# Kernel tuning notes

Hardware: AMD Instinct MI355X
Metric: run time of the kernel (lower is better)

## Reference

```python
import jax, jax.numpy as jnp
import numpy as np

B, L, D = 8, 8192, 1024
M = L // 4  # target_ratio=4 -> exactly L/4 boundaries per batch row (enforced in setup_inputs)


@jax.custom_vjp
def ste(x):
    # Forward: ones_like(x). Backward: pass gradient straight through.
    return jnp.ones_like(x)

def _ste_fwd(x):
    return jnp.ones_like(x), None

def _ste_bwd(_, g):
    return (g,)

ste.defvjp(_ste_fwd, _ste_bwd)


def _ema_combine(c1, c2):
    # Linear recurrence h = a*h_prev + b as an associative op (matches the
    # Hillis-Steele doubling scan in the torch source exactly).
    a1, b1 = c1
    a2, b2 = c2
    return (a1 * a2, a2[..., None] * b1 + b2)


def setup_inputs() -> dict:
    key = jax.random.key(0)
    k1, k2, k3, k4, k5 = jax.random.split(key, 5)
    x = jax.random.normal(k1, (B, L, D), jnp.float32)
    residual = jax.random.normal(k2, (B, L, D), jnp.float32)
    prob = jax.random.uniform(k3, (B, L), jnp.float32)
    # exactly M=L//4 True positions per row (random locations) -> static M
    r = jax.random.uniform(k4, (B, L))
    sel = jnp.argsort(r, axis=1)[:, :M]
    token_mask = jnp.zeros((B, L), bool).at[jnp.arange(B)[:, None], sel].set(True)
    state = jax.random.normal(k5, (B, D), jnp.float32)
    return {"x": x, "residual": residual, "prob": prob,
            "token_mask": token_mask, "state": state}


def reference(x, residual, prob, token_mask, state):
    # ---- Tokenizer: compact selected positions to the front (stable order) ----
    counts = token_mask.sum(axis=1)                       # (B,)
    order = jnp.argsort(~token_mask, axis=1)[:, :M]       # stable: True positions first, in order
    chunked = jnp.take_along_axis(x, order[:, :, None], axis=1)      # (B, M, D)
    chunk_probs = jnp.take_along_axis(prob, order, axis=1)           # (B, M)
    valid = jnp.arange(M)[None, :] < counts[:, None]                  # (B, M)
    chunk_probs = chunk_probs * valid                     # padded slots -> 0 (new_zeros semantics)

    # ---- EMA scan over compacted chunks ----
    decay = jnp.clip(1.0 - chunk_probs, 0.0, 1.0)         # (B, M)
    b = (1.0 - decay)[..., None] * chunked                # (B, M, D)
    b = b.at[:, 0].add(decay[:, 0, None] * state)         # fold initial state into b[0]
    _, ema = jax.lax.associative_scan(_ema_combine, (decay, b), axis=1)
    ema = ema * valid[..., None]

    # ---- DeTokenizer: scatter-expand back to (B, L, D) ----
    chunk_idx = jnp.cumsum(token_mask.astype(jnp.int32), axis=1) - 1  # (B, L)
    valid_pos = chunk_idx >= 0
    ci = jnp.clip(chunk_idx, 0, M - 1)
    long_states = jnp.take_along_axis(ema, ci[:, :, None], axis=1)    # (B, L, D)
    long_states = long_states * valid_pos[..., None]

    coef = ste(jnp.maximum(1.0 - prob, prob))             # forward: ones; bwd: STE
    long_states = long_states * coef[..., None]

    output = residual + long_states                       # (B, L, D)

    # new_state = last valid EMA value per batch (or carried-over state if empty)
    last = jnp.clip(counts - 1, 0, M - 1)
    new_state = jnp.take_along_axis(ema, last[:, None, None], axis=1)[:, 0]
    new_state = jnp.where((counts > 0)[:, None], new_state, state)
    return output, new_state
```

## Files before the change

kernel.cpp:

```cpp
#include <hip/hip_runtime.h>
#include <stdint.h>
#include <stddef.h>

#define B_ 8
#define L_ 8192
#define D_ 1024
#define M_ 2048
#define D4_ (D_/4)
#define TROWS_ 64
#define NTILE_ (L_/TROWS_)

typedef float f4 __attribute__((ext_vector_type(4)));

#define OFF_POS    ((size_t)0)
#define OFF_DEC    (OFF_POS  + (size_t)B_*M_*4)
#define OFF_A      (OFF_DEC  + (size_t)B_*M_*4)
#define OFF_CIT    (OFF_A    + (size_t)B_*NTILE_*4)
#define OFF_EZ     (OFF_CIT  + (size_t)B_*NTILE_*4)
#define OFF_HINIT  (OFF_EZ   + (size_t)B_*NTILE_*D_*4)
#define WS_TOTAL   (OFF_HINIT + (size_t)B_*NTILE_*D_*4)

__global__ __launch_bounds__(1024)
void compact_kernel(const void* __restrict__ mask_raw,
                    const float* __restrict__ prob,
                    int* __restrict__ pos,
                    float* __restrict__ dec,
                    int* __restrict__ ci_tile) {
    const int b = blockIdx.x;
    const int t = threadIdx.x;

    __shared__ int u8flag;
    if (t == 0) u8flag = 0;
    __syncthreads();
    {
        const uint32_t* mu = (const uint32_t*)mask_raw;
        uint32_t w0 = mu[t * 2], w1 = mu[t * 2 + 1];
        if (w0 > 1u || w1 > 1u) atomicOr(&u8flag, 1);
    }
    __syncthreads();
    const bool u8 = (u8flag != 0);

    int mv[8];
    const int base_l = t * 8;
    if (u8) {
        const uint8_t* mrow = (const uint8_t*)mask_raw + (size_t)b * L_;
        #pragma unroll
        for (int j = 0; j < 8; j++) mv[j] = mrow[base_l + j] ? 1 : 0;
    } else {
        const int* mrow = (const int*)mask_raw + (size_t)b * L_;
        #pragma unroll
        for (int j = 0; j < 8; j++) mv[j] = mrow[base_l + j] ? 1 : 0;
    }
    int tsum = 0;
    #pragma unroll
    for (int j = 0; j < 8; j++) tsum += mv[j];

    const int lane = t & 63, wid = t >> 6;
    int v = tsum;
    #pragma unroll
    for (int off = 1; off < 64; off <<= 1) {
        int n = __shfl_up(v, off, 64);
        if (lane >= off) v += n;
    }
    __shared__ int wsum[16];
    __shared__ int woff[16];
    if (lane == 63) wsum[wid] = v;
    __syncthreads();
    if (t < 16) {
        int acc = 0;
        for (int w = 0; w < t; w++) acc += wsum[w];
        woff[t] = acc;
    }
    __syncthreads();
    int run = (v - tsum) + woff[wid];

    const float* prow = prob + (size_t)b * L_;
    #pragma unroll
    for (int j = 0; j < 8; j++) {
        const int l = base_l + j;
        if (mv[j]) {
            float d = 1.0f - prow[l];
            d = fminf(fmaxf(d, 0.0f), 1.0f);
            pos[(size_t)b * M_ + run] = l;
            dec[(size_t)b * M_ + run] = d;
            run += 1;
        }
    }
    if ((t & 7) == 7) {
        const int k = (t + 1) >> 3;
        if (k < NTILE_) ci_tile[b * NTILE_ + k] = run - 1;
    }
}

__global__ __launch_bounds__(256)
void segend_kernel(const f4* __restrict__ x4,
                   const int* __restrict__ pos,
                   const float* __restrict__ dec,
                   const int* __restrict__ ci_tile,
                   f4* __restrict__ ez4,
                   float* __restrict__ Aseg) {
    const int blk = blockIdx.x;
    const int b = blk >> 7;
    const int k = blk & (NTILE_ - 1);
    const int t = threadIdx.x;

    const int mlo = (k == 0) ? 0 : ci_tile[b * NTILE_ + k] + 1;
    const int mhi = (k == NTILE_ - 1) ? (M_ - 1) : ci_tile[b * NTILE_ + k + 1];
    const int n = mhi - mlo + 1;

    __shared__ int   pl[TROWS_];
    __shared__ float dl[TROWS_];
    if (t < n) {
        pl[t] = pos[(size_t)b * M_ + mlo + t];
        dl[t] = dec[(size_t)b * M_ + mlo + t];
    }
    __syncthreads();

    f4 h = (f4)(0.0f);
    float A = 1.0f;
    if (n > 0) {
        const f4* xrow = x4 + (size_t)b * L_ * D4_;
        for (int g = 0; g < n; g += 8) {
            f4    xv[8];
            float dd[8];
            #pragma unroll
            for (int j = 0; j < 8; j++) {
                const int mm = g + j;
                const int mc = (mm < n) ? mm : 0;
                dd[j] = (mm < n) ? dl[mc] : 1.0f;
                xv[j] = xrow[(size_t)pl[mc] * D4_ + t];
            }
            #pragma unroll
            for (int j = 0; j < 8; j++) {
                h = dd[j] * h + (1.0f - dd[j]) * xv[j];
                A *= dd[j];
            }
        }
    }
    ez4[(size_t)blk * D4_ + t] = h;
    if (t == 0) Aseg[blk] = A;
}

__global__ __launch_bounds__(64)
void combine_kernel(const float* __restrict__ ez,
                    const float* __restrict__ Aseg,
                    const float* __restrict__ state,
                    float* __restrict__ hinit,
                    float* __restrict__ newstate) {
    const int b = blockIdx.x;
    const int ch = blockIdx.y * 64 + threadIdx.x;
    __shared__ float Al[NTILE_];
    for (int i = threadIdx.x; i < NTILE_; i += 64) Al[i] = Aseg[b * NTILE_ + i];
    __syncthreads();

    float c = state[(size_t)b * D_ + ch];
    for (int s0 = 0; s0 < NTILE_; s0 += 8) {
        float e[8];
        #pragma unroll
        for (int j = 0; j < 8; j++)
            e[j] = ez[((size_t)b * NTILE_ + s0 + j) * D_ + ch];
        #pragma unroll
        for (int j = 0; j < 8; j++) {
            hinit[((size_t)b * NTILE_ + s0 + j) * D_ + ch] = c;
            c = fmaf(Al[s0 + j], c, e[j]);
        }
    }
    newstate[(size_t)b * D_ + ch] = c;
}

__global__ __launch_bounds__(256)
void fused_kernel(const f4* __restrict__ x4,
                  const f4* __restrict__ res4,
                  const int* __restrict__ pos,
                  const float* __restrict__ dec,
                  const int* __restrict__ ci_tile,
                  const f4* __restrict__ hinit4,
                  f4* __restrict__ out4) {
    const int blk = blockIdx.x;
    const int b = blk >> 7;
    const int k = blk & (NTILE_ - 1);
    const int t = threadIdx.x;
    const int l0 = k * TROWS_;

    const int m0 = (k == 0) ? -1 : ci_tile[b * NTILE_ + k];

    __shared__ int   pl[TROWS_ + 2];
    __shared__ float dl[TROWS_ + 2];
    if (t < TROWS_ + 2) {
        const int mm = m0 + 1 + t;
        if (mm < M_) {
            pl[t] = pos[(size_t)b * M_ + mm];
            dl[t] = dec[(size_t)b * M_ + mm];
        } else {
            pl[t] = L_;
            dl[t] = 1.0f;
        }
    }
    __syncthreads();

    const f4* xrow = x4 + (size_t)b * L_ * D4_;

    f4 h = hinit4[(size_t)blk * D4_ + t];
    float live = (m0 >= 0) ? 1.0f : 0.0f;

    const f4* resrow = res4 + (size_t)b * L_ * D4_;
    f4*       outrow = out4 + (size_t)b * L_ * D4_;

    int mi = 0;
    int nextb = pl[0];
    int a0 = (pl[0] < L_) ? pl[0] : 0;
    int a1 = (pl[1] < L_) ? pl[1] : 0;
    f4 xn  = xrow[(size_t)a0 * D4_ + t];
    f4 xn2 = xrow[(size_t)a1 * D4_ + t];
    int l = l0;

    #define ADV(K, HH, LV)                                                \
        if (l + (K) == nextb) {                                           \
            const float d_ = dl[mi];                                      \
            h = d_ * h + (1.0f - d_) * xn;                                \
            live = 1.0f;                                                  \
            xn = xn2;                                                     \
            ++mi;                                                         \
            nextb = pl[mi];                                               \
            const int nr_ = (pl[mi + 1] < L_) ? pl[mi + 1] : 0;           \
            xn2 = xrow[(size_t)nr_ * D4_ + t];                            \
        }                                                                 \
        HH = h; LV = live;

    f4 c0, c1, c2, c3;
    c0 = __builtin_nontemporal_load(resrow + (size_t)(l + 0) * D4_ + t);
    c1 = __builtin_nontemporal_load(resrow + (size_t)(l + 1) * D4_ + t);
    c2 = __builtin_nontemporal_load(resrow + (size_t)(l + 2) * D4_ + t);
    c3 = __builtin_nontemporal_load(resrow + (size_t)(l + 3) * D4_ + t);
    for (int g = 0; g < (TROWS_ / 4) - 1; ++g) {
        f4 n0 = __builtin_nontemporal_load(resrow + (size_t)(l + 4) * D4_ + t);
        f4 n1 = __builtin_nontemporal_load(resrow + (size_t)(l + 5) * D4_ + t);
        f4 n2 = __builtin_nontemporal_load(resrow + (size_t)(l + 6) * D4_ + t);
        f4 n3 = __builtin_nontemporal_load(resrow + (size_t)(l + 7) * D4_ + t);
        f4 h0, h1, h2, h3;
        float v0, v1, v2, v3;
        ADV(0, h0, v0); ADV(1, h1, v1); ADV(2, h2, v2); ADV(3, h3, v3);
        __builtin_nontemporal_store(c0 + v0 * h0, outrow + (size_t)(l + 0) * D4_ + t);
        __builtin_nontemporal_store(c1 + v1 * h1, outrow + (size_t)(l + 1) * D4_ + t);
        __builtin_nontemporal_store(c2 + v2 * h2, outrow + (size_t)(l + 2) * D4_ + t);
        __builtin_nontemporal_store(c3 + v3 * h3, outrow + (size_t)(l + 3) * D4_ + t);
        c0 = n0; c1 = n1; c2 = n2; c3 = n3;
        l += 4;
    }
    {
        f4 h0, h1, h2, h3;
        float v0, v1, v2, v3;
        ADV(0, h0, v0); ADV(1, h1, v1); ADV(2, h2, v2); ADV(3, h3, v3);
        __builtin_nontemporal_store(c0 + v0 * h0, outrow + (size_t)(l + 0) * D4_ + t);
        __builtin_nontemporal_store(c1 + v1 * h1, outrow + (size_t)(l + 1) * D4_ + t);
        __builtin_nontemporal_store(c2 + v2 * h2, outrow + (size_t)(l + 2) * D4_ + t);
        __builtin_nontemporal_store(c3 + v3 * h3, outrow + (size_t)(l + 3) * D4_ + t);
    }
    #undef ADV
}

extern "C" void kernel_launch(void* const* d_in, const int* in_sizes, int n_in,
                              void* d_out, int out_size, void* d_ws, size_t ws_size,
                              hipStream_t stream) {
    const float* x        = (const float*)d_in[0];
    const float* residual = (const float*)d_in[1];
    const float* prob     = (const float*)d_in[2];
    const void*  mask     = d_in[3];
    const float* state    = (const float*)d_in[4];

    float* out       = (float*)d_out;
    float* new_state = out + (size_t)B_ * L_ * D_;

    if (ws_size < WS_TOTAL) return;

    char* ws = (char*)d_ws;
    int*   pos     = (int*)  (ws + OFF_POS);
    float* dec     = (float*)(ws + OFF_DEC);
    float* Aseg    = (float*)(ws + OFF_A);
    int*   ci_tile = (int*)  (ws + OFF_CIT);
    float* ez      = (float*)(ws + OFF_EZ);
    float* hinit   = (float*)(ws + OFF_HINIT);

    compact_kernel<<<B_, 1024, 0, stream>>>(mask, prob, pos, dec, ci_tile);

    segend_kernel<<<B_ * NTILE_, 256, 0, stream>>>(
        (const f4*)x, pos, dec, ci_tile, (f4*)ez, Aseg);

    combine_kernel<<<dim3(B_, 16), 64, 0, stream>>>(
        ez, Aseg, state, hinit, new_state);

    fused_kernel<<<B_ * NTILE_, 256, 0, stream>>>(
        (const f4*)x, (const f4*)residual, pos, dec, ci_tile,
        (const f4*)hinit, (f4*)out);
}
```

Before: 134.9 us.

## Fuse four-stage pipeline into one cooperative kernel with grid syncs

Replaces the four separate launches (compact, segment-end scan, tile combine, fused output) with a single cooperative mega-kernel of 1024 blocks that separates the phases with grid.sync. The separate kernels are kept as a fallback if the cooperative launch fails. The goal is to remove launch gaps and inter-kernel drain between phases. In exchange, most blocks sit idle during the compact and combine phases, and each grid barrier has its own cost. The compaction phase also now runs with 256 threads per row instead of 1024.

After: 481.2 us. 257% more time.

```diff
diff --git a/kernel.cpp b/kernel.cpp
--- a/kernel.cpp
+++ b/kernel.cpp
@@ -1,6 +1,9 @@
 #include <hip/hip_runtime.h>
+#include <hip/hip_cooperative_groups.h>
 #include <stdint.h>
 #include <stddef.h>
+
+namespace cg = cooperative_groups;
 
 #define B_ 8
 #define L_ 8192
@@ -9,6 +12,7 @@
 #define D4_ (D_/4)
 #define TROWS_ 64
 #define NTILE_ (L_/TROWS_)
+#define NBLK_ (B_*NTILE_)
 
 typedef float f4 __attribute__((ext_vector_type(4)));
 
@@ -20,172 +24,111 @@
 #define OFF_HINIT  (OFF_EZ   + (size_t)B_*NTILE_*D_*4)
 #define WS_TOTAL   (OFF_HINIT + (size_t)B_*NTILE_*D_*4)
 
-__global__ __launch_bounds__(1024)
-void compact_kernel(const void* __restrict__ mask_raw,
-                    const float* __restrict__ prob,
-                    int* __restrict__ pos,
-                    float* __restrict__ dec,
-                    int* __restrict__ ci_tile) {
-    const int b = blockIdx.x;
+__global__ __launch_bounds__(256, 4)
+void mega_kernel(const f4* __restrict__ x4,
+                 const f4* __restrict__ res4,
+                 const float* __restrict__ prob,
+                 const void* __restrict__ mask_raw,
+                 const float* __restrict__ state,
+                 int* __restrict__ pos,
+                 float* __restrict__ dec,
+                 float* __restrict__ Aseg,
+                 int* __restrict__ ci_tile,
+                 float* __restrict__ ez,
+                 float* __restrict__ hinit,
+                 f4* __restrict__ out4,
+                 float* __restrict__ newstate) {
+    cg::grid_group grid = cg::this_grid();
+    const int blk = blockIdx.x;
     const int t = threadIdx.x;
 
-    __shared__ int u8flag;
-    if (t == 0) u8flag = 0;
-    __syncthreads();
-    {
-        const uint32_t* mu = (const uint32_t*)mask_raw;
-        uint32_t w0 = mu[t * 2], w1 = mu[t * 2 + 1];
-        if (w0 > 1u || w1 > 1u) atomicOr(&u8flag, 1);
-    }
-    __syncthreads();
-    const bool u8 = (u8flag != 0);
-
-    int mv[8];
-    const int base_l = t * 8;
-    if (u8) {
-        const uint8_t* mrow = (const uint8_t*)mask_raw + (size_t)b * L_;
+    __shared__ int   u8flag;
+    __shared__ int   wsum[4];
+    __shared__ int   woff[4];
+    __shared__ int   pl[TROWS_ + 2];
+    __shared__ float dl[TROWS_ + 2];
+    __shared__ float Al[NTILE_];
+
+    if (blk < B_) {
+        const int b = blk;
+        if (t == 0) u8flag = 0;
+        __syncthreads();
+        {
+            const uint32_t* mu = (const uint32_t*)mask_raw;
+            uint32_t orv = 0;
+            #pragma unroll
+            for (int j = 0; j < 8; j++) orv |= mu[t * 8 + j];
+            if (orv > 1u) atomicOr(&u8flag, 1);
+        }
+        __syncthreads();
+        const bool u8 = (u8flag != 0);
+
+        const int base_l = t * 32;
+        int cnt = 0;
+        if (u8) {
+            const uint8_t* mrow = (const uint8_t*)mask_raw + (size_t)b * L_;
+            #pragma unroll
+            for (int j = 0; j < 32; j++) cnt += mrow[base_l + j] ? 1 : 0;
+        } else {
+            const int* mrow = (const int*)mask_raw + (size_t)b * L_;
+            #pragma unroll
+            for (int j = 0; j < 32; j++) cnt += mrow[base_l + j] ? 1 : 0;
+        }
+        const int lane = t & 63, wid = t >> 6;
+        int v = cnt;
         #pragma unroll
-        for (int j = 0; j < 8; j++) mv[j] = mrow[base_l + j] ? 1 : 0;
-    } else {
-        const int* mrow = (const int*)mask_raw + (size_t)b * L_;
-        #pragma unroll
-        for (int j = 0; j < 8; j++) mv[j] = mrow[base_l + j] ? 1 : 0;
-    }
-    int tsum = 0;
-    #pragma unroll
-    for (int j = 0; j < 8; j++) tsum += mv[j];
-
-    const int lane = t & 63, wid = t >> 6;
-    int v = tsum;
-    #pragma unroll
-    for (int off = 1; off < 64; off <<= 1) {
-        int n = __shfl_up(v, off, 64);
-        if (lane >= off) v += n;
-    }
-    __shared__ int wsum[16];
-    __shared__ int woff[16];
-    if (lane == 63) wsum[wid] = v;
-    __syncthreads();
-    if (t < 16) {
-        int acc = 0;
-        for (int w = 0; w < t; w++) acc += wsum[w];
-        woff[t] = acc;
-    }
-    __syncthreads();
-    int run = (v - tsum) + woff[wid];
-
-    const float* prow = prob + (size_t)b * L_;
-    #pragma unroll
-    for (int j = 0; j < 8; j++) {
-        const int l = base_l + j;
-        if (mv[j]) {
-            float d = 1.0f - prow[l];
-            d = fminf(fmaxf(d, 0.0f), 1.0f);
-            pos[(size_t)b * M_ + run] = l;
-            dec[(size_t)b * M_ + run] = d;
-            run += 1;
-        }
-    }
-    if ((t & 7) == 7) {
-        const int k = (t + 1) >> 3;
-        if (k < NTILE_) ci_tile[b * NTILE_ + k] = run - 1;
-    }
-}
-
-__global__ __launch_bounds__(256)
-void segend_kernel(const f4* __restrict__ x4,
-                   const int* __restrict__ pos,
-                   const float* __restrict__ dec,
-                   const int* __restrict__ ci_tile,
-                   f4* __restrict__ ez4,
-                   float* __restrict__ Aseg) {
-    const int blk = blockIdx.x;
+        for (int off = 1; off < 64; off <<= 1) {
+            int n = __shfl_up(v, off, 64);
+            if (lane >= off) v += n;
+        }
+        if (lane == 63) wsum[wid] = v;
+        __syncthreads();
+        if (t < 4) {
+            int acc = 0;
+            for (int w = 0; w < t; w++) acc += wsum[w];
+            woff[t] = acc;
+        }
+        __syncthreads();
+        int run = (v - cnt) + woff[wid];
+
+        const float* prow = prob + (size_t)b * L_;
+        if (u8) {
+            const uint8_t* mrow = (const uint8_t*)mask_raw + (size_t)b * L_;
+            for (int j = 0; j < 32; j++) {
+                const int l = base_l + j;
+                if (mrow[l]) {
+                    float d = fminf(fmaxf(1.0f - prow[l], 0.0f), 1.0f);
+                    pos[(size_t)b * M_ + run] = l;
+                    dec[(size_t)b * M_ + run] = d;
+                    run++;
+                }
+            }
+        } else {
+            const int* mrow = (const int*)mask_raw + (size_t)b * L_;
+            for (int j = 0; j < 32; j++) {
+                const int l = base_l + j;
+                if (mrow[l]) {
+                    float d = fminf(fmaxf(1.0f - prow[l], 0.0f), 1.0f);
+                    pos[(size_t)b * M_ + run] = l;
+                    dec[(size_t)b * M_ + run] = d;
+                    run++;
+                }
+            }
+        }
+        if (t & 1) {
+            const int k = (t + 1) >> 1;
+            if (k < NTILE_) ci_tile[b * NTILE_ + k] = run - 1;
+        }
+        __threadfence();
+    }
+    grid.sync();
+
     const int b = blk >> 7;
     const int k = blk & (NTILE_ - 1);
-    const int t = threadIdx.x;
-
-    const int mlo = (k == 0) ? 0 : ci_tile[b * NTILE_ + k] + 1;
+    const int m0 = (k == 0) ? -1 : ci_tile[b * NTILE_ + k];
     const int mhi = (k == NTILE_ - 1) ? (M_ - 1) : ci_tile[b * NTILE_ + k + 1];
-    const int n = mhi - mlo + 1;
-
-    __shared__ int   pl[TROWS_];
-    __shared__ float dl[TROWS_];
-    if (t < n) {
-        pl[t] = pos[(size_t)b * M_ + mlo + t];
-        dl[t] = dec[(size_t)b * M_ + mlo + t];
-    }
-    __syncthreads();
-
-    f4 h = (f4)(0.0f);
-    float A = 1.0f;
-    if (n > 0) {
-        const f4* xrow = x4 + (size_t)b * L_ * D4_;
-        for (int g = 0; g < n; g += 8) {
-            f4    xv[8];
-            float dd[8];
-            #pragma unroll
-            for (int j = 0; j < 8; j++) {
-                const int mm = g + j;
-                const int mc = (mm < n) ? mm : 0;
-                dd[j] = (mm < n) ? dl[mc] : 1.0f;
-                xv[j] = xrow[(size_t)pl[mc] * D4_ + t];
-            }
-            #pragma unroll
-            for (int j = 0; j < 8; j++) {
-                h = dd[j] * h + (1.0f - dd[j]) * xv[j];
-                A *= dd[j];
-            }
-        }
-    }
-    ez4[(size_t)blk * D4_ + t] = h;
-    if (t == 0) Aseg[blk] = A;
-}
-
-__global__ __launch_bounds__(64)
-void combine_kernel(const float* __restrict__ ez,
-                    const float* __restrict__ Aseg,
-                    const float* __restrict__ state,
-                    float* __restrict__ hinit,
-                    float* __restrict__ newstate) {
-    const int b = blockIdx.x;
-    const int ch = blockIdx.y * 64 + threadIdx.x;
-    __shared__ float Al[NTILE_];
-    for (int i = threadIdx.x; i < NTILE_; i += 64) Al[i] = Aseg[b * NTILE_ + i];
-    __syncthreads();
-
-    float c = state[(size_t)b * D_ + ch];
-    for (int s0 = 0; s0 < NTILE_; s0 += 8) {
-        float e[8];
-        #pragma unroll
-        for (int j = 0; j < 8; j++)
-            e[j] = ez[((size_t)b * NTILE_ + s0 + j) * D_ + ch];
-        #pragma unroll
-        for (int j = 0; j < 8; j++) {
-            hinit[((size_t)b * NTILE_ + s0 + j) * D_ + ch] = c;
-            c = fmaf(Al[s0 + j], c, e[j]);
-        }
-    }
-    newstate[(size_t)b * D_ + ch] = c;
-}
-
-__global__ __launch_bounds__(256)
-void fused_kernel(const f4* __restrict__ x4,
-                  const f4* __restrict__ res4,
-                  const int* __restrict__ pos,
-                  const float* __restrict__ dec,
-                  const int* __restrict__ ci_tile,
-                  const f4* __restrict__ hinit4,
-                  f4* __restrict__ out4) {
-    const int blk = blockIdx.x;
-    const int b = blk >> 7;
-    const int k = blk & (NTILE_ - 1);
-    const int t = threadIdx.x;
-    const int l0 = k * TROWS_;
-
-    const int m0 = (k == 0) ? -1 : ci_tile[b * NTILE_ + k];
-
-    __shared__ int   pl[TROWS_ + 2];
-    __shared__ float dl[TROWS_ + 2];
+    const int n = mhi - m0;
+
     if (t < TROWS_ + 2) {
         const int mm = m0 + 1 + t;
         if (mm < M_) {
@@ -199,8 +142,55 @@
     __syncthreads();
 
     const f4* xrow = x4 + (size_t)b * L_ * D4_;
-
-    f4 h = hinit4[(size_t)blk * D4_ + t];
+    {
+        f4 h = (f4)(0.0f);
+        float A = 1.0f;
+        for (int g = 0; g < n; g += 8) {
+            f4    xv[8];
+            float dd[8];
+            #pragma unroll
+            for (int j = 0; j < 8; j++) {
+                const int mm = g + j;
+                const int mc = (mm < n) ? mm : 0;
+                dd[j] = (mm < n) ? dl[mc] : 1.0f;
+                xv[j] = xrow[(size_t)pl[mc] * D4_ + t];
+            }
+            #pragma unroll
+            for (int j = 0; j < 8; j++) {
+                h = dd[j] * h + (1.0f - dd[j]) * xv[j];
+                A *= dd[j];
+            }
+        }
+        ((f4*)ez)[(size_t)blk * D4_ + t] = h;
+        if (t == 0) Aseg[blk] = A;
+    }
+    __threadfence();
+    grid.sync();
+
+    if (blk < 32) {
+        const int b2 = blk >> 2;
+        const int ch = ((blk & 3) << 8) + t;
+        for (int i = t; i < NTILE_; i += 256) Al[i] = Aseg[b2 * NTILE_ + i];
+        __syncthreads();
+        float c = state[(size_t)b2 * D_ + ch];
+        for (int s0 = 0; s0 < NTILE_; s0 += 8) {
+            float e[8];
+            #pragma unroll
+            for (int j = 0; j < 8; j++)
+                e[j] = ez[((size_t)b2 * NTILE_ + s0 + j) * D_ + ch];
+            #pragma unroll
+            for (int j = 0; j < 8; j++) {
+                hinit[((size_t)b2 * NTILE_ + s0 + j) * D_ + ch] = c;
+                c = fmaf(Al[s0 + j], c, e[j]);
+            }
+        }
+        newstate[(size_t)b2 * D_ + ch] = c;
+        __threadfence();
+    }
+    grid.sync();
+
+    const int l0 = k * TROWS_;
+    f4 h = ((const f4*)hinit)[(size_t)blk * D4_ + t];
     float live = (m0 >= 0) ? 1.0f : 0.0f;
 
     const f4* resrow = res4 + (size_t)b * L_ * D4_;
@@ -259,6 +249,228 @@
     #undef ADV
 }
 
+__global__ __launch_bounds__(1024)
+void compact_kernel(const void* __restrict__ mask_raw,
+                    const float* __restrict__ prob,
+                    int* __restrict__ pos,
+                    float* __restrict__ dec,
+                    int* __restrict__ ci_tile) {
+    const int b = blockIdx.x;
+    const int t = threadIdx.x;
+    __shared__ int u8flag;
+    if (t == 0) u8flag = 0;
+    __syncthreads();
+    {
+        const uint32_t* mu = (const uint32_t*)mask_raw;
+        uint32_t w0 = mu[t * 2], w1 = mu[t * 2 + 1];
+        if (w0 > 1u || w1 > 1u) atomicOr(&u8flag, 1);
+    }
+    __syncthreads();
+    const bool u8 = (u8flag != 0);
+    int mv[8];
+    const int base_l = t * 8;
+    if (u8) {
+        const uint8_t* mrow = (const uint8_t*)mask_raw + (size_t)b * L_;
+        #pragma unroll
+        for (int j = 0; j < 8; j++) mv[j] = mrow[base_l + j] ? 1 : 0;
+    } else {
+        const int* mrow = (const int*)mask_raw + (size_t)b * L_;
+        #pragma unroll
+        for (int j = 0; j < 8; j++) mv[j] = mrow[base_l + j] ? 1 : 0;
+    }
+    int tsum = 0;
+    #pragma unroll
+    for (int j = 0; j < 8; j++) tsum += mv[j];
+    const int lane = t & 63, wid = t >> 6;
+    int v = tsum;
+    #pragma unroll
+    for (int off = 1; off < 64; off <<= 1) {
+        int n = __shfl_up(v, off, 64);
+        if (lane >= off) v += n;
+    }
+    __shared__ int wsum[16];
+    __shared__ int woff[16];
+    if (lane == 63) wsum[wid] = v;
+    __syncthreads();
+    if (t < 16) {
+        int acc = 0;
+        for (int w = 0; w < t; w++) acc += wsum[w];
+        woff[t] = acc;
+    }
+    __syncthreads();
+    int run = (v - tsum) + woff[wid];
+    const float* prow = prob + (size_t)b * L_;
+    #pragma unroll
+    for (int j = 0; j < 8; j++) {
+        const int l = base_l + j;
+        if (mv[j]) {
+            float d = fminf(fmaxf(1.0f - prow[l], 0.0f), 1.0f);
+            pos[(size_t)b * M_ + run] = l;
+            dec[(size_t)b * M_ + run] = d;
+            run += 1;
+        }
+    }
+    if ((t & 7) == 7) {
+        const int k = (t + 1) >> 3;
+        if (k < NTILE_) ci_tile[b * NTILE_ + k] = run - 1;
+    }
+}
+
+__global__ __launch_bounds__(256)
+void segend_kernel(const f4* __restrict__ x4,
+                   const int* __restrict__ pos,
+                   const float* __restrict__ dec,
+                   const int* __restrict__ ci_tile,
+                   f4* __restrict__ ez4,
+                   float* __restrict__ Aseg) {
+    const int blk = blockIdx.x;
+    const int b = blk >> 7;
+    const int k = blk & (NTILE_ - 1);
+    const int t = threadIdx.x;
+    const int mlo = (k == 0) ? 0 : ci_tile[b * NTILE_ + k] + 1;
+    const int mhi = (k == NTILE_ - 1) ? (M_ - 1) : ci_tile[b * NTILE_ + k + 1];
+    const int n = mhi - mlo + 1;
+    __shared__ int   pl[TROWS_];
+    __shared__ float dl[TROWS_];
+    if (t < n) {
+        pl[t] = pos[(size_t)b * M_ + mlo + t];
+        dl[t] = dec[(size_t)b * M_ + mlo + t];
+    }
+    __syncthreads();
+    f4 h = (f4)(0.0f);
+    float A = 1.0f;
+    if (n > 0) {
+        const f4* xrow = x4 + (size_t)b * L_ * D4_;
+        for (int g = 0; g < n; g += 8) {
+            f4    xv[8];
+            float dd[8];
+            #pragma unroll
+            for (int j = 0; j < 8; j++) {
+                const int mm = g + j;
+                const int mc = (mm < n) ? mm : 0;
+                dd[j] = (mm < n) ? dl[mc] : 1.0f;
+                xv[j] = xrow[(size_t)pl[mc] * D4_ + t];
+            }
+            #pragma unroll
+            for (int j = 0; j < 8; j++) {
+                h = dd[j] * h + (1.0f - dd[j]) * xv[j];
+                A *= dd[j];
+            }
+        }
+    }
+    ez4[(size_t)blk * D4_ + t] = h;
+    if (t == 0) Aseg[blk] = A;
+}
+
+__global__ __launch_bounds__(64)
+void combine_kernel(const float* __restrict__ ez,
+                    const float* __restrict__ Aseg,
+                    const float* __restrict__ state,
+                    float* __restrict__ hinit,
+                    float* __restrict__ newstate) {
+    const int b = blockIdx.x;
+    const int ch = blockIdx.y * 64 + threadIdx.x;
+    __shared__ float Al[NTILE_];
+    for (int i = threadIdx.x; i < NTILE_; i += 64) Al[i] = Aseg[b * NTILE_ + i];
+    __syncthreads();
+    float c = state[(size_t)b * D_ + ch];
+    for (int s0 = 0; s0 < NTILE_; s0 += 8) {
+        float e[8];
+        #pragma unroll
+        for (int j = 0; j < 8; j++)
+            e[j] = ez[((size_t)b * NTILE_ + s0 + j) * D_ + ch];
+        #pragma unroll
+        for (int j = 0; j < 8; j++) {
+            hinit[((size_t)b * NTILE_ + s0 + j) * D_ + ch] = c;
+            c = fmaf(Al[s0 + j], c, e[j]);
+        }
+    }
+    newstate[(size_t)b * D_ + ch] = c;
+}
+
+__global__ __launch_bounds__(256)
+void fused_kernel(const f4* __restrict__ x4,
+                  const f4* __restrict__ res4,
+                  const int* __restrict__ pos,
+                  const float* __restrict__ dec,
+                  const int* __restrict__ ci_tile,
+                  const f4* __restrict__ hinit4,
+                  f4* __restrict__ out4) {
+    const int blk = blockIdx.x;
+    const int b = blk >> 7;
+    const int k = blk & (NTILE_ - 1);
+    const int t = threadIdx.x;
+    const int l0 = k * TROWS_;
+    const int m0 = (k == 0) ? -1 : ci_tile[b * NTILE_ + k];
+    __shared__ int   pl[TROWS_ + 2];
+    __shared__ float dl[TROWS_ + 2];
+    if (t < TROWS_ + 2) {
+        const int mm = m0 + 1 + t;
+        if (mm < M_) {
+            pl[t] = pos[(size_t)b * M_ + mm];
+            dl[t] = dec[(size_t)b * M_ + mm];
+        } else {
+            pl[t] = L_;
+            dl[t] = 1.0f;
+        }
+    }
+    __syncthreads();
+    const f4* xrow = x4 + (size_t)b * L_ * D4_;
+    f4 h = hinit4[(size_t)blk * D4_ + t];
+    float live = (m0 >= 0) ? 1.0f : 0.0f;
+    const f4* resrow = res4 + (size_t)b * L_ * D4_;
+    f4*       outrow = out4 + (size_t)b * L_ * D4_;
+    int mi = 0;
+    int nextb = pl[0];
+    int a0 = (pl[0] < L_) ? pl[0] : 0;
+    int a1 = (pl[1] < L_) ? pl[1] : 0;
+    f4 xn  = xrow[(size_t)a0 * D4_ + t];
+    f4 xn2 = xrow[(size_t)a1 * D4_ + t];
+    int l = l0;
+    #define ADV(K, HH, LV)                                                \
+        if (l + (K) == nextb) {                                           \
+            const float d_ = dl[mi];                                      \
+            h = d_ * h + (1.0f - d_) * xn;                                \
+            live = 1.0f;                                                  \
+            xn = xn2;                                                     \
+            ++mi;                                                         \
+            nextb = pl[mi];                                               \
+            const int nr_ = (pl[mi + 1] < L_) ? pl[mi + 1] : 0;           \
+            xn2 = xrow[(size_t)nr_ * D4_ + t];                            \
+        }                                                                 \
+        HH = h; LV = live;
+    f4 c0, c1, c2, c3;
+    c0 = __builtin_nontemporal_load(resrow + (size_t)(l + 0) * D4_ + t);
+    c1 = __builtin_nontemporal_load(resrow + (size_t)(l + 1) * D4_ + t);
+    c2 = __builtin_nontemporal_load(resrow + (size_t)(l + 2) * D4_ + t);
+    c3 = __builtin_nontemporal_load(resrow + (size_t)(l + 3) * D4_ + t);
+    for (int g = 0; g < (TROWS_ / 4) - 1; ++g) {
+        f4 n0 = __builtin_nontemporal_load(resrow + (size_t)(l + 4) * D4_ + t);
+        f4 n1 = __builtin_nontemporal_load(resrow + (size_t)(l + 5) * D4_ + t);
+        f4 n2 = __builtin_nontemporal_load(resrow + (size_t)(l + 6) * D4_ + t);
+        f4 n3 = __builtin_nontemporal_load(resrow + (size_t)(l + 7) * D4_ + t);
+        f4 h0, h1, h2, h3;
+        float v0, v1, v2, v3;
+        ADV(0, h0, v0); ADV(1, h1, v1); ADV(2, h2, v2); ADV(3, h3, v3);
+        __builtin_nontemporal_store(c0 + v0 * h0, outrow + (size_t)(l + 0) * D4_ + t);
+        __builtin_nontemporal_store(c1 + v1 * h1, outrow + (size_t)(l + 1) * D4_ + t);
+        __builtin_nontemporal_store(c2 + v2 * h2, outrow + (size_t)(l + 2) * D4_ + t);
+        __builtin_nontemporal_store(c3 + v3 * h3, outrow + (size_t)(l + 3) * D4_ + t);
+        c0 = n0; c1 = n1; c2 = n2; c3 = n3;
+        l += 4;
+    }
+    {
+        f4 h0, h1, h2, h3;
+        float v0, v1, v2, v3;
+        ADV(0, h0, v0); ADV(1, h1, v1); ADV(2, h2, v2); ADV(3, h3, v3);
+        __builtin_nontemporal_store(c0 + v0 * h0, outrow + (size_t)(l + 0) * D4_ + t);
+        __builtin_nontemporal_store(c1 + v1 * h1, outrow + (size_t)(l + 1) * D4_ + t);
+        __builtin_nontemporal_store(c2 + v2 * h2, outrow + (size_t)(l + 2) * D4_ + t);
+        __builtin_nontemporal_store(c3 + v3 * h3, outrow + (size_t)(l + 3) * D4_ + t);
+    }
+    #undef ADV
+}
+
 extern "C" void kernel_launch(void* const* d_in, const int* in_sizes, int n_in,
                               void* d_out, int out_size, void* d_ws, size_t ws_size,
                               hipStream_t stream) {
@@ -281,15 +493,22 @@
     float* ez      = (float*)(ws + OFF_EZ);
     float* hinit   = (float*)(ws + OFF_HINIT);
 
-    compact_kernel<<<B_, 1024, 0, stream>>>(mask, prob, pos, dec, ci_tile);
-
-    segend_kernel<<<B_ * NTILE_, 256, 0, stream>>>(
-        (const f4*)x, pos, dec, ci_tile, (f4*)ez, Aseg);
-
-    combine_kernel<<<dim3(B_, 16), 64, 0, stream>>>(
-        ez, Aseg, state, hinit, new_state);
-
-    fused_kernel<<<B_ * NTILE_, 256, 0, stream>>>(
-        (const f4*)x, (const f4*)residual, pos, dec, ci_tile,
-        (const f4*)hinit, (f4*)out);
+    const f4* x4   = (const f4*)x;
+    const f4* res4 = (const f4*)residual;
+    f4*       out4 = (f4*)out;
+
+    void* args[] = {
+        (void*)&x4, (void*)&res4, (void*)&prob, (void*)&mask, (void*)&state,
+        (void*)&pos, (void*)&dec, (void*)&Aseg, (void*)&ci_tile,
+        (void*)&ez, (void*)&hinit, (void*)&out4, (void*)&new_state
+    };
+    hipError_t err = hipLaunchCooperativeKernel(
+        (const void*)mega_kernel, dim3(NBLK_), dim3(256), args, 0, stream);
+
+    if (err != hipSuccess) {
+        compact_kernel<<<B_, 1024, 0, stream>>>(mask, prob, pos, dec, ci_tile);
+        segend_kernel<<<B_ * NTILE_, 256, 0, stream>>>(x4, pos, dec, ci_tile, (f4*)ez, Aseg);
+        combine_kernel<<<dim3(B_, 16), 64, 0, stream>>>(ez, Aseg, state, hinit, new_state);
+        fused_kernel<<<B_ * NTILE_, 256, 0, stream>>>(x4, res4, pos, dec, ci_tile, (const f4*)hinit, out4);
+    }
 }
```
